# Optimization experiments

Measured on AMD Instinct MI355X. Metric: run time of the kernel, lower is better.

Reference implementation:

```python
import jax, jax.numpy as jnp
import numpy as np

B, T = 8192, 26
V, E, H, L = 23, 100, 128, 64  # vocab, emb dim, GRU hidden, latent; LSTM hidden = E


def setup_inputs() -> dict:
    key = jax.random.key(0)
    ks = jax.random.split(key, 16)
    rn = lambda k, shape, scale=0.1: (jax.random.normal(k, shape, jnp.float32) * scale)
    emb = rn(ks[0], (V, E)).at[0].set(0.0)  # padding_idx=0 row zeroed
    return {
        "z": jax.random.normal(ks[1], (B, L), jnp.float32),
        "x_in": jax.random.randint(ks[2], (B, T), 0, V),
        "emb": emb,
        "fc_z_w": rn(ks[3], (H, L)), "fc_z_b": rn(ks[4], (H,)),
        "gru_wih": rn(ks[5], (3 * H, E)), "gru_whh": rn(ks[6], (3 * H, H)),
        "gru_bih": rn(ks[7], (3 * H,)), "gru_bhh": rn(ks[8], (3 * H,)),
        "lstm_wih": rn(ks[9], (4 * E, H)), "lstm_whh": rn(ks[10], (4 * E, E)),
        "lstm_bih": rn(ks[11], (4 * E,)), "lstm_bhh": rn(ks[12], (4 * E,)),
        "out_w": rn(ks[13], (V, E)), "out_b": rn(ks[14], (V,)),
    }


def _gru(e, h0, Wih, Whh, bih, bhh):
    # e: (B,T,E); precompute input projections for all steps, scan over T.
    xg = jnp.einsum('bti,gi->btg', e, Wih) + bih  # (B,T,3H)

    def step(h, x):
        hg = h @ Whh.T + bhh
        xr, xz, xn = jnp.split(x, 3, axis=-1)
        hr, hz, hn = jnp.split(hg, 3, axis=-1)
        r = jax.nn.sigmoid(xr + hr)
        zg = jax.nn.sigmoid(xz + hz)
        n = jnp.tanh(xn + r * hn)
        h_new = (1.0 - zg) * n + zg * h
        return h_new, h_new

    _, ys = jax.lax.scan(step, h0, jnp.swapaxes(xg, 0, 1))  # (T,B,H)
    return jnp.swapaxes(ys, 0, 1)


def _lstm(x, h0, c0, Wih, Whh, bih, bhh):
    xg = jnp.einsum('bti,gi->btg', x, Wih) + bih  # (B,T,4E)

    def step(hc, xt):
        h, c = hc
        g = xt + h @ Whh.T + bhh
        i, f, gg, o = jnp.split(g, 4, axis=-1)
        c_new = jax.nn.sigmoid(f) * c + jax.nn.sigmoid(i) * jnp.tanh(gg)
        h_new = jax.nn.sigmoid(o) * jnp.tanh(c_new)
        return (h_new, c_new), h_new

    _, ys = jax.lax.scan(step, (h0, c0), jnp.swapaxes(xg, 0, 1))
    return jnp.swapaxes(ys, 0, 1)


def reference(z, x_in, emb, fc_z_w, fc_z_b, gru_wih, gru_whh, gru_bih, gru_bhh,
              lstm_wih, lstm_whh, lstm_bih, lstm_bhh, out_w, out_b):
    h0 = jnp.tanh(z @ fc_z_w.T + fc_z_b)            # (B,H)
    e = emb[x_in]                                    # (B,T,E)
    y = _gru(e, h0, gru_wih, gru_whh, gru_bih, gru_bhh)           # (B,T,H)
    zeros = jnp.zeros((z.shape[0], E), dtype=z.dtype)
    y = _lstm(y, zeros, zeros, lstm_wih, lstm_whh, lstm_bih, lstm_bhh)  # (B,T,E)
    logits = jnp.einsum('bte,ve->btv', y, out_w) + out_b          # (B,T,V)
    return logits
```

## Files before the change

kernel.cpp:

```cpp
#include <hip/hip_runtime.h>
#include <stdint.h>
#include <stddef.h>

#define BB 8192
#define TT 26
#define VV 23
#define EE 100
#define HH 128
#define LL 64

typedef __attribute__((ext_vector_type(8))) short bf16x8;
typedef __attribute__((ext_vector_type(4))) float f32x4;

#define MFMA(a, b, c) __builtin_amdgcn_mfma_f32_16x16x32_bf16((a), (b), (c), 0, 0, 0)

#define OFF_GRUW   0ull
#define OFF_TBL    98304ull
#define OFF_LSTMW  122880ull
#define OFF_OUTW   352256ull
#define OFF_FCZW   360448ull
#define OFF_LBIAS  376832ull

#define L_LW    0
#define L_HF    114688
#define L_LH    131072
#define L_IDX   147456
#define L_TOTAL 148480

__device__ __forceinline__ void force_frag(bf16x8& v) { asm volatile("" : "+v"(v)); }

__device__ __forceinline__ unsigned short f2bf(float f) {
  union { float f; unsigned u; } v; v.f = f;
  unsigned u = v.u;
  return (unsigned short)((u + 0x7FFFu + ((u >> 16) & 1u)) >> 16);
}
__device__ __forceinline__ unsigned short f2bf_fast(float f) {
  union { float f; unsigned u; } v; v.f = f;
  return (unsigned short)((v.u + 0x8000u) >> 16);
}
#define LOG2E 1.4426950408889634f
__device__ __forceinline__ float sigm(float x) {
  return __builtin_amdgcn_rcpf(1.0f + __builtin_amdgcn_exp2f(-x * LOG2E));
}
__device__ __forceinline__ float tanh_(float x) {
  return __builtin_fmaf(-2.0f,
      __builtin_amdgcn_rcpf(1.0f + __builtin_amdgcn_exp2f(x * (2.0f * LOG2E))), 1.0f);
}

__global__ __launch_bounds__(256) void prep_kernel(
    const float* __restrict__ fc_z_w, const float* __restrict__ gru_whh,
    const float* __restrict__ lstm_wih, const float* __restrict__ lstm_whh,
    const float* __restrict__ lstm_bih, const float* __restrict__ lstm_bhh,
    const float* __restrict__ out_w,
    const float* __restrict__ emb, const float* __restrict__ gru_wih,
    const float* __restrict__ gru_bih, const float* __restrict__ gru_bhh,
    char* __restrict__ ws)
{
  __shared__ float emb_s[VV * EE];
  __shared__ float wih_s[16 * EE];
  __shared__ float bih_s[16];
  const int blk = blockIdx.x;
  const int tid = threadIdx.x;

  if (blk >= 690) {
    const int blk2 = blk - 690;
    const int ct   = blk2 >> 1;
    const int half = blk2 & 1;
    const int n0   = ct * 16;

    for (int i = tid; i < VV * EE; i += 256) emb_s[i] = emb[i];
    for (int i = tid; i < 16 * EE; i += 256) wih_s[i] = gru_wih[n0 * EE + i];
    if (tid < 16) bih_s[tid] = gru_bih[n0 + tid];
    __syncthreads();

    const int t512 = half * 256 + tid;
    const int j    = t512 & 7;
    const int lane = (t512 >> 3) & 63;
    const int n16  = lane & 15;
    const int k    = ((lane >> 4) & 3) * 8 + j;
    const int g    = ct >> 3;
    float v = 0.0f;
    if (k < VV) {
      const float* ep = emb_s + k * EE;
      const float* wp = wih_s + n16 * EE;
      float s0 = 0.f, s1 = 0.f, s2 = 0.f, s3 = 0.f;
#pragma unroll 5
      for (int m = 0; m < EE; m += 4) {
        s0 += ep[m] * wp[m];         s1 += ep[m + 1] * wp[m + 1];
        s2 += ep[m + 2] * wp[m + 2]; s3 += ep[m + 3] * wp[m + 3];
      }
      v = bih_s[n16] + ((s0 + s1) + (s2 + s3));
      if (g < 2) v += gru_bhh[g * HH + (ct & 7) * 16 + n16];
    }
    *(unsigned short*)(ws + OFF_TBL + (size_t)(ct * 512 + t512) * 2) = f2bf(v);
    return;
  }

  int e = blk * 256 + tid;

  if (e < 49152) {
    int j = e & 7, lane = (e >> 3) & 63, kc = (e >> 9) & 3, ct = e >> 11;
    int n = ct * 16 + (lane & 15);
    int k = kc * 32 + ((lane >> 4) & 3) * 8 + j;
    *(unsigned short*)(ws + OFF_GRUW + (size_t)e * 2) = f2bf(gru_whh[n * HH + k]);
    return;
  }
  e -= 49152;
  if (e < 114688) {
    int j = e & 7, lane = (e >> 3) & 63, kc = (e >> 9) & 7, ct = e >> 12;
    int row = ct * 16 + (lane & 15);
    int g = row / 112, c = row % 112;
    int q = (lane >> 4) & 3;
    float v = 0.0f;
    if (c < EE) {
      if (kc < 4) {
        int k = kc * 32 + q * 8 + j;
        v = lstm_wih[(g * EE + c) * HH + k];
      } else {
        int k = (kc - 4) * 32 + q * 8 + j;
        if (k < EE) v = lstm_whh[(g * EE + c) * EE + k];
      }
    }
    *(unsigned short*)(ws + OFF_LSTMW + (size_t)e * 2) = f2bf(v);
    return;
  }
  e -= 114688;
  if (e < 4096) {
    int j = e & 7, lane = (e >> 3) & 63, kc = (e >> 9) & 3, ct = e >> 11;
    int n = ct * 16 + (lane & 15);
    int k = kc * 32 + ((lane >> 4) & 3) * 8 + j;
    float v = (n < VV && k < EE) ? out_w[n * EE + k] : 0.0f;
    *(unsigned short*)(ws + OFF_OUTW + (size_t)e * 2) = f2bf(v);
    return;
  }
  e -= 4096;
  if (e < 8192) {
    int j = e & 7, lane = (e >> 3) & 63, kc = (e >> 9) & 1, ct = e >> 10;
    int n = ct * 16 + (lane & 15);
    int k = kc * 32 + ((lane >> 4) & 3) * 8 + j;
    *(unsigned short*)(ws + OFF_FCZW + (size_t)e * 2) = f2bf(fc_z_w[n * LL + k]);
    return;
  }
  e -= 8192;
  if (e < 448) {
    int g = e / 112, c = e % 112;
    float v = (c < EE) ? (lstm_bih[g * EE + c] + lstm_bhh[g * EE + c]) : 0.0f;
    *(float*)(ws + OFF_LBIAS + (size_t)e * 4) = v;
  }
}

__global__ __launch_bounds__(1024, 4) void fused_kernel(
    const float* __restrict__ z, const int* __restrict__ x_in,
    const float* __restrict__ fc_z_b, const float* __restrict__ gru_bhh,
    const unsigned short* __restrict__ gruw, const unsigned short* __restrict__ tbl,
    const unsigned short* __restrict__ fczw,
    const unsigned short* __restrict__ lstmw, const float* __restrict__ lbias,
    const float* __restrict__ out_b, const unsigned short* __restrict__ outw,
    float* __restrict__ out)
{
  extern __shared__ char smem[];
  unsigned short* lwlds = (unsigned short*)(smem + L_LW);
  char*           hfrag = smem + L_HF;
  char*           lhbuf = smem + L_LH;
  unsigned char*  idx_lds = (unsigned char*)(smem + L_IDX);

  const int tid  = threadIdx.x;
  const int wv   = tid >> 6;
  const int lane = tid & 63;
  const int l15  = lane & 15;
  const int q    = (lane >> 4) & 3;
  const int blk  = blockIdx.x;

  for (int i = tid; i < 8192; i += 1024)
    ((unsigned short*)lhbuf)[i] = 0;
  for (int f = tid; f < 7168; f += 1024) {
    int frag_i = f >> 6, within = f & 63;
    int ct = frag_i >> 2, kcl = frag_i & 3;
    *(bf16x8*)((char*)lwlds + (size_t)frag_i * 1024 + within * 16) =
        *(const bf16x8*)(lstmw + ((size_t)(ct * 8 + 4 + kcl)) * 512 + within * 8);
  }

  if (wv < 8) {
    {
      int rid = wv * 64 + lane;
      for (int i = rid; i < TT * 32; i += 512) {
        int t = i >> 5, r = i & 31;
        idx_lds[i] = (unsigned char)x_in[(blk * 32 + r) * TT + t];
      }
    }
    bf16x8 gw[3][4], tw[3];
#pragma unroll
    for (int g = 0; g < 3; g++) {
      int ct = g * 8 + wv;
#pragma unroll
      for (int kc = 0; kc < 4; kc++) {
        gw[g][kc] = *(const bf16x8*)(gruw + (size_t)(ct * 4 + kc) * 512 + lane * 8);
        force_frag(gw[g][kc]);
      }
      tw[g] = *(const bf16x8*)(tbl + (size_t)ct * 512 + lane * 8);
      force_frag(tw[g]);
    }
    const int col = wv * 16 + l15;
    const float b_n = gru_bhh[2 * HH + col];
    const int wbase = (col >> 5) * 512 + ((col >> 3) & 3) * 128 + (col & 7);

    float h[2][4];
    {
      bf16x8 fw0 = *(const bf16x8*)(fczw + (size_t)(wv * 2 + 0) * 512 + lane * 8);
      bf16x8 fw1 = *(const bf16x8*)(fczw + (size_t)(wv * 2 + 1) * 512 + lane * 8);
      float fzb = fc_z_b[col];
#pragma unroll
      for (int mt = 0; mt < 2; mt++) {
        const float* zp = z + (size_t)(blk * 32 + mt * 16 + l15) * LL + q * 8;
        f32x4 z0 = *(const f32x4*)(zp);
        f32x4 z1 = *(const f32x4*)(zp + 4);
        f32x4 z2 = *(const f32x4*)(zp + 32);
        f32x4 z3 = *(const f32x4*)(zp + 36);
        bf16x8 za0, za1;
#pragma unroll
        for (int j = 0; j < 4; j++) {
          za0[j]     = (short)f2bf(z0[j]);
          za0[4 + j] = (short)f2bf(z1[j]);
          za1[j]     = (short)f2bf(z2[j]);
          za1[4 + j] = (short)f2bf(z3[j]);
        }
        f32x4 acc = {fzb, fzb, fzb, fzb};
        acc = MFMA(za0, fw0, acc);
        acc = MFMA(za1, fw1, acc);
#pragma unroll
        for (int i = 0; i < 4; i++) {
          h[mt][i] = tanh_(acc[i]);
          ((unsigned short*)(hfrag + mt * 4096))[wbase + (q * 4 + i) * 8]
              = f2bf_fast(h[mt][i]);
        }
      }
    }
    __syncthreads();

    for (int p = 0; p < TT + 2; p++) {
      if (p < TT) {
#pragma unroll
        for (int mt = 0; mt < 2; mt++) {
          int iv = idx_lds[p * 32 + mt * 16 + l15];
          bf16x8 oh;
#pragma unroll
          for (int j = 0; j < 8; j++)
            oh[j] = (short)((iv == q * 8 + j) ? 0x3F80 : 0);

          f32x4 ar  = {0.0f, 0.0f, 0.0f, 0.0f};
          f32x4 az  = {0.0f, 0.0f, 0.0f, 0.0f};
          f32x4 ahn = {b_n, b_n, b_n, b_n};
          f32x4 axn = {0.0f, 0.0f, 0.0f, 0.0f};
          ar  = MFMA(oh, tw[0], ar);
          az  = MFMA(oh, tw[1], az);
          axn = MFMA(oh, tw[2], axn);

          bf16x8 a[4];
#pragma unroll
          for (int kc = 0; kc < 4; kc++)
            a[kc] = *(const bf16x8*)(hfrag + (p & 1) * 8192 + mt * 4096
                                     + kc * 1024 + lane * 16);
#pragma unroll
          for (int kc = 0; kc < 4; kc++) {
            ar  = MFMA(a[kc], gw[0][kc], ar);
            az  = MFMA(a[kc], gw[1][kc], az);
            ahn = MFMA(a[kc], gw[2][kc], ahn);
          }
#pragma unroll
          for (int i = 0; i < 4; i++) {
            float r  = sigm(ar[i]);
            float zg = sigm(az[i]);
            float n  = tanh_(__builtin_fmaf(r, ahn[i], axn[i]));
            h[mt][i] = __builtin_fmaf(zg, h[mt][i] - n, n);
            ((unsigned short*)(hfrag + ((p + 1) & 1) * 8192 + mt * 4096))
                [wbase + (q * 4 + i) * 8] = f2bf_fast(h[mt][i]);
          }
        }
      }
      __syncthreads();
    }
  } else if (wv < 15) {
    const int tile = wv - 8;
    bf16x8 lwy[4][3];
#pragma unroll
    for (int g = 0; g < 4; g++)
#pragma unroll
      for (int kc = 0; kc < 3; kc++) {
        lwy[g][kc] = *(const bf16x8*)(lstmw + (size_t)((g * 7 + tile) * 8 + kc) * 512 + lane * 8);
        force_frag(lwy[g][kc]);
      }
    const int col = tile * 16 + l15;
    float b[4];
#pragma unroll
    for (int g = 0; g < 4; g++) b[g] = lbias[g * 112 + col];
    const int wbase = (col >> 5) * 512 + ((col >> 3) & 3) * 128 + (col & 7);
    float c[2][4] = {{0, 0, 0, 0}, {0, 0, 0, 0}};
    __syncthreads();

    for (int p = 0; p < TT + 2; p++) {
      if (p >= 1 && p <= TT) {
        bf16x8 yw3[4];
#pragma unroll
        for (int g = 0; g < 4; g++)
          yw3[g] = *(const bf16x8*)(lstmw + (size_t)((g * 7 + tile) * 8 + 3) * 512 + lane * 8);

        f32x4 acc[2][4];
#pragma unroll
        for (int mt = 0; mt < 2; mt++)
#pragma unroll
          for (int g = 0; g < 4; g++) {
            f32x4 ini = {b[g], b[g], b[g], b[g]};
            acc[mt][g] = ini;
          }

#pragma unroll
        for (int kc = 0; kc < 3; kc++) {
          bf16x8 ya0 = *(const bf16x8*)(hfrag + (p & 1) * 8192 + 0 * 4096
                                        + kc * 1024 + lane * 16);
          bf16x8 ya1 = *(const bf16x8*)(hfrag + (p & 1) * 8192 + 1 * 4096
                                        + kc * 1024 + lane * 16);
#pragma unroll
          for (int g = 0; g < 4; g++) {
            acc[0][g] = MFMA(ya0, lwy[g][kc], acc[0][g]);
            acc[1][g] = MFMA(ya1, lwy[g][kc], acc[1][g]);
          }
        }
        {
          bf16x8 ya0 = *(const bf16x8*)(hfrag + (p & 1) * 8192 + 0 * 4096
                                        + 3 * 1024 + lane * 16);
          bf16x8 ya1 = *(const bf16x8*)(hfrag + (p & 1) * 8192 + 1 * 4096
                                        + 3 * 1024 + lane * 16);
#pragma unroll
          for (int g = 0; g < 4; g++) {
            acc[0][g] = MFMA(ya0, yw3[g], acc[0][g]);
            acc[1][g] = MFMA(ya1, yw3[g], acc[1][g]);
          }
        }
#pragma unroll
        for (int kc = 0; kc < 4; kc++) {
          const char* wb = (const char*)lwlds + (size_t)(tile * 4 + kc) * 1024 + lane * 16;
          bf16x8 w0 = *(const bf16x8*)(wb);
          bf16x8 w1 = *(const bf16x8*)(wb + 28672);
          bf16x8 w2 = *(const bf16x8*)(wb + 2 * 28672);
          bf16x8 w3 = *(const bf16x8*)(wb + 3 * 28672);
          bf16x8 ha0 = *(const bf16x8*)(lhbuf + ((p - 1) & 1) * 8192 + 0 * 4096
                                        + kc * 1024 + lane * 16);
          bf16x8 ha1 = *(const bf16x8*)(lhbuf + ((p - 1) & 1) * 8192 + 1 * 4096
                                        + kc * 1024 + lane * 16);
          acc[0][0] = MFMA(ha0, w0, acc[0][0]);
          acc[0][1] = MFMA(ha0, w1, acc[0][1]);
          acc[0][2] = MFMA(ha0, w2, acc[0][2]);
          acc[0][3] = MFMA(ha0, w3, acc[0][3]);
          acc[1][0] = MFMA(ha1, w0, acc[1][0]);
          acc[1][1] = MFMA(ha1, w1, acc[1][1]);
          acc[1][2] = MFMA(ha1, w2, acc[1][2]);
          acc[1][3] = MFMA(ha1, w3, acc[1][3]);
        }
#pragma unroll
        for (int mt = 0; mt < 2; mt++) {
#pragma unroll
          for (int i = 0; i < 4; i++) {
            float ii = sigm(acc[mt][0][i]), ff = sigm(acc[mt][1][i]);
            float gg = tanh_(acc[mt][2][i]), oo = sigm(acc[mt][3][i]);
            float cn = __builtin_fmaf(ff, c[mt][i], ii * gg);
            c[mt][i] = cn;
            ((unsigned short*)(lhbuf + (p & 1) * 8192 + mt * 4096))
                [wbase + (q * 4 + i) * 8] = f2bf_fast(oo * tanh_(cn));
          }
        }
      }
      __syncthreads();
    }
  } else {
    bf16x8 ow[2][4];
#pragma unroll
    for (int ct = 0; ct < 2; ct++)
#pragma unroll
      for (int kc = 0; kc < 4; kc++) {
        ow[ct][kc] = *(const bf16x8*)(outw + (size_t)(ct * 4 + kc) * 512 + lane * 8);
        force_frag(ow[ct][kc]);
      }
    float ob[2];
#pragma unroll
    for (int ct = 0; ct < 2; ct++) {
      int cv = ct * 16 + l15;
      ob[ct] = (cv < VV) ? out_b[cv] : 0.0f;
    }
    __syncthreads();

    for (int p = 0; p < TT + 2; p++) {
      if (p >= 2) {
        const int t = p - 2;
#pragma unroll
        for (int mt = 0; mt < 2; mt++) {
          bf16x8 ha[4];
#pragma unroll
          for (int kc = 0; kc < 4; kc++)
            ha[kc] = *(const bf16x8*)(lhbuf + ((p - 1) & 1) * 8192 + mt * 4096
                                      + kc * 1024 + lane * 16);
#pragma unroll
          for (int ct = 0; ct < 2; ct++) {
            f32x4 acc = {ob[ct], ob[ct], ob[ct], ob[ct]};
#pragma unroll
            for (int kc = 0; kc < 4; kc++)
              acc = MFMA(ha[kc], ow[ct][kc], acc);
            int cv = ct * 16 + l15;
            if (cv < VV) {
#pragma unroll
              for (int i = 0; i < 4; i++) {
                int rowg = blk * 32 + mt * 16 + q * 4 + i;
                out[((size_t)rowg * TT + t) * VV + cv] = acc[i];
              }
            }
          }
        }
      }
      __syncthreads();
    }
  }
}

extern "C" void kernel_launch(void* const* d_in, const int* in_sizes, int n_in,
                              void* d_out, int out_size, void* d_ws, size_t ws_size,
                              hipStream_t stream) {
  (void)in_sizes; (void)n_in; (void)out_size; (void)ws_size;
  const float* z        = (const float*)d_in[0];
  const int*   x_in     = (const int*)  d_in[1];
  const float* emb      = (const float*)d_in[2];
  const float* fc_z_w   = (const float*)d_in[3];
  const float* fc_z_b   = (const float*)d_in[4];
  const float* gru_wih  = (const float*)d_in[5];
  const float* gru_whh  = (const float*)d_in[6];
  const float* gru_bih  = (const float*)d_in[7];
  const float* gru_bhh  = (const float*)d_in[8];
  const float* lstm_wih = (const float*)d_in[9];
  const float* lstm_whh = (const float*)d_in[10];
  const float* lstm_bih = (const float*)d_in[11];
  const float* lstm_bhh = (const float*)d_in[12];
  const float* out_w    = (const float*)d_in[13];
  const float* out_b    = (const float*)d_in[14];
  char*  ws  = (char*)d_ws;
  float* out = (float*)d_out;

  const unsigned short* gruw  = (const unsigned short*)(ws + OFF_GRUW);
  const unsigned short* tblp  = (const unsigned short*)(ws + OFF_TBL);
  const unsigned short* lstmw = (const unsigned short*)(ws + OFF_LSTMW);
  const unsigned short* outw  = (const unsigned short*)(ws + OFF_OUTW);
  const unsigned short* fczw  = (const unsigned short*)(ws + OFF_FCZW);
  const float*          lbias = (const float*)(ws + OFF_LBIAS);

  hipFuncSetAttribute((const void*)fused_kernel,
                      hipFuncAttributeMaxDynamicSharedMemorySize, L_TOTAL);

  prep_kernel<<<738, 256, 0, stream>>>(fc_z_w, gru_whh, lstm_wih, lstm_whh,
                                       lstm_bih, lstm_bhh, out_w,
                                       emb, gru_wih, gru_bih, gru_bhh, ws);
  fused_kernel<<<256, 1024, L_TOTAL, stream>>>(z, x_in, fc_z_b, gru_bhh,
                                               gruw, tblp, fczw, lstmw, lbias,
                                               out_b, outw, out);
}
```

Baseline: 185.9 us.

## Replace per-step block barriers with LDS counters and triple-buffered states

Replaces the per-timestep __syncthreads between the GRU, LSTM and output warp groups with LDS atomic counters (wait/post) and moves the GRU and LSTM hidden-state buffers from double to triple buffering. The aim is to let the pipeline stages drift relative to each other instead of running in lockstep, so one slow stage does not stall every warp. The LSTM y-weights are now held fully in registers, and fewer recurrent-weight fragments are staged in LDS, with the last K chunk read from global memory each step. This adds spin-wait overhead, the risk of a subtle ordering bug, and extra register pressure.

```diff
diff --git a/kernel.cpp b/kernel.cpp
--- a/kernel.cpp
+++ b/kernel.cpp
@@ -22,10 +22,11 @@
 #define OFF_LBIAS  376832ull
 
 #define L_LW    0
-#define L_HF    114688
-#define L_LH    131072
-#define L_IDX   147456
-#define L_TOTAL 148480
+#define L_HF    86016
+#define L_LH    110592
+#define L_IDX   135168
+#define L_CNT   136192
+#define L_TOTAL 136448
 
 __device__ __forceinline__ void force_frag(bf16x8& v) { asm volatile("" : "+v"(v)); }
 
@@ -45,6 +46,17 @@
 __device__ __forceinline__ float tanh_(float x) {
   return __builtin_fmaf(-2.0f,
       __builtin_amdgcn_rcpf(1.0f + __builtin_amdgcn_exp2f(x * (2.0f * LOG2E))), 1.0f);
+}
+
+__device__ __forceinline__ void wait_ge(int* cnt, int tgt) {
+  while (__hip_atomic_load(cnt, __ATOMIC_ACQUIRE, __HIP_MEMORY_SCOPE_WORKGROUP) < tgt)
+    __builtin_amdgcn_s_sleep(2);
+  __builtin_amdgcn_sched_barrier(0);
+}
+__device__ __forceinline__ void post_cnt(int* cnt, int lane) {
+  __threadfence_block();
+  if (lane == 0)
+    __hip_atomic_fetch_add(cnt, 1, __ATOMIC_RELEASE, __HIP_MEMORY_SCOPE_WORKGROUP);
 }
 
 __global__ __launch_bounds__(256) void prep_kernel(
@@ -163,6 +175,10 @@
   char*           hfrag = smem + L_HF;
   char*           lhbuf = smem + L_LH;
   unsigned char*  idx_lds = (unsigned char*)(smem + L_IDX);
+  int*            cnts  = (int*)(smem + L_CNT);
+  int* cg = cnts + 0;
+  int* cl = cnts + 16;
+  int* co = cnts + 32;
 
   const int tid  = threadIdx.x;
   const int wv   = tid >> 6;
@@ -171,11 +187,12 @@
   const int q    = (lane >> 4) & 3;
   const int blk  = blockIdx.x;
 
-  for (int i = tid; i < 8192; i += 1024)
+  if (tid < 48) cnts[tid] = 0;
+  for (int i = tid; i < 12288; i += 1024)
     ((unsigned short*)lhbuf)[i] = 0;
-  for (int f = tid; f < 7168; f += 1024) {
+  for (int f = tid; f < 5376; f += 1024) {
     int frag_i = f >> 6, within = f & 63;
-    int ct = frag_i >> 2, kcl = frag_i & 3;
+    int ct = frag_i / 3, kcl = frag_i % 3;
     *(bf16x8*)((char*)lwlds + (size_t)frag_i * 1024 + within * 16) =
         *(const bf16x8*)(lstmw + ((size_t)(ct * 8 + 4 + kcl)) * 512 + within * 8);
   }
@@ -230,15 +247,20 @@
 #pragma unroll
         for (int i = 0; i < 4; i++) {
           h[mt][i] = tanh_(acc[i]);
-          ((unsigned short*)(hfrag + mt * 4096))[wbase + (q * 4 + i) * 8]
+          ((unsigned short*)(hfrag + 2 * 8192 + mt * 4096))[wbase + (q * 4 + i) * 8]
               = f2bf_fast(h[mt][i]);
         }
       }
     }
     __syncthreads();
 
+#pragma unroll 1
     for (int p = 0; p < TT + 2; p++) {
+      wait_ge(cg, 8 * p);
+      if (p >= 3 && p < TT) wait_ge(cl, 7 * (p - 1));
       if (p < TT) {
+        const int br = (p + 2) % 3;
+        const int bw = (p + 3) % 3;
 #pragma unroll
         for (int mt = 0; mt < 2; mt++) {
           int iv = idx_lds[p * 32 + mt * 16 + l15];
@@ -258,7 +280,7 @@
           bf16x8 a[4];
 #pragma unroll
           for (int kc = 0; kc < 4; kc++)
-            a[kc] = *(const bf16x8*)(hfrag + (p & 1) * 8192 + mt * 4096
+            a[kc] = *(const bf16x8*)(hfrag + br * 8192 + mt * 4096
                                      + kc * 1024 + lane * 16);
 #pragma unroll
           for (int kc = 0; kc < 4; kc++) {
@@ -272,20 +294,20 @@
             float zg = sigm(az[i]);
             float n  = tanh_(__builtin_fmaf(r, ahn[i], axn[i]));
             h[mt][i] = __builtin_fmaf(zg, h[mt][i] - n, n);
-            ((unsigned short*)(hfrag + ((p + 1) & 1) * 8192 + mt * 4096))
+            ((unsigned short*)(hfrag + bw * 8192 + mt * 4096))
                 [wbase + (q * 4 + i) * 8] = f2bf_fast(h[mt][i]);
           }
         }
       }
-      __syncthreads();
+      post_cnt(cg, lane);
     }
   } else if (wv < 15) {
     const int tile = wv - 8;
-    bf16x8 lwy[4][3];
+    bf16x8 lwy[4][4];
 #pragma unroll
     for (int g = 0; g < 4; g++)
 #pragma unroll
-      for (int kc = 0; kc < 3; kc++) {
+      for (int kc = 0; kc < 4; kc++) {
         lwy[g][kc] = *(const bf16x8*)(lstmw + (size_t)((g * 7 + tile) * 8 + kc) * 512 + lane * 8);
         force_frag(lwy[g][kc]);
       }
@@ -297,79 +319,66 @@
     float c[2][4] = {{0, 0, 0, 0}, {0, 0, 0, 0}};
     __syncthreads();
 
+#pragma unroll 1
     for (int p = 0; p < TT + 2; p++) {
+      wait_ge(cl, 7 * p);
       if (p >= 1 && p <= TT) {
-        bf16x8 yw3[4];
-#pragma unroll
-        for (int g = 0; g < 4; g++)
-          yw3[g] = *(const bf16x8*)(lstmw + (size_t)((g * 7 + tile) * 8 + 3) * 512 + lane * 8);
-
-        f32x4 acc[2][4];
-#pragma unroll
-        for (int mt = 0; mt < 2; mt++)
+        wait_ge(cg, 8 * p);
+        if (p >= 4) wait_ge(co, p - 1);
+        const int by = (p + 2) % 3;
+        const int bh = (p + 1) % 3;
+        const int bw2 = (p + 2) % 3;
+#pragma unroll
+        for (int mt = 0; mt < 2; mt++) {
+          f32x4 acc[4];
 #pragma unroll
           for (int g = 0; g < 4; g++) {
             f32x4 ini = {b[g], b[g], b[g], b[g]};
-            acc[mt][g] = ini;
-          }
-
-#pragma unroll
-        for (int kc = 0; kc < 3; kc++) {
-          bf16x8 ya0 = *(const bf16x8*)(hfrag + (p & 1) * 8192 + 0 * 4096
-                                        + kc * 1024 + lane * 16);
-          bf16x8 ya1 = *(const bf16x8*)(hfrag + (p & 1) * 8192 + 1 * 4096
-                                        + kc * 1024 + lane * 16);
-#pragma unroll
-          for (int g = 0; g < 4; g++) {
-            acc[0][g] = MFMA(ya0, lwy[g][kc], acc[0][g]);
-            acc[1][g] = MFMA(ya1, lwy[g][kc], acc[1][g]);
-          }
-        }
-        {
-          bf16x8 ya0 = *(const bf16x8*)(hfrag + (p & 1) * 8192 + 0 * 4096
-                                        + 3 * 1024 + lane * 16);
-          bf16x8 ya1 = *(const bf16x8*)(hfrag + (p & 1) * 8192 + 1 * 4096
-                                        + 3 * 1024 + lane * 16);
-#pragma unroll
-          for (int g = 0; g < 4; g++) {
-            acc[0][g] = MFMA(ya0, yw3[g], acc[0][g]);
-            acc[1][g] = MFMA(ya1, yw3[g], acc[1][g]);
-          }
-        }
-#pragma unroll
-        for (int kc = 0; kc < 4; kc++) {
-          const char* wb = (const char*)lwlds + (size_t)(tile * 4 + kc) * 1024 + lane * 16;
-          bf16x8 w0 = *(const bf16x8*)(wb);
-          bf16x8 w1 = *(const bf16x8*)(wb + 28672);
-          bf16x8 w2 = *(const bf16x8*)(wb + 2 * 28672);
-          bf16x8 w3 = *(const bf16x8*)(wb + 3 * 28672);
-          bf16x8 ha0 = *(const bf16x8*)(lhbuf + ((p - 1) & 1) * 8192 + 0 * 4096
-                                        + kc * 1024 + lane * 16);
-          bf16x8 ha1 = *(const bf16x8*)(lhbuf + ((p - 1) & 1) * 8192 + 1 * 4096
-                                        + kc * 1024 + lane * 16);
-          acc[0][0] = MFMA(ha0, w0, acc[0][0]);
-          acc[0][1] = MFMA(ha0, w1, acc[0][1]);
-          acc[0][2] = MFMA(ha0, w2, acc[0][2]);
-          acc[0][3] = MFMA(ha0, w3, acc[0][3]);
-          acc[1][0] = MFMA(ha1, w0, acc[1][0]);
-          acc[1][1] = MFMA(ha1, w1, acc[1][1]);
-          acc[1][2] = MFMA(ha1, w2, acc[1][2]);
-          acc[1][3] = MFMA(ha1, w3, acc[1][3]);
-        }
-#pragma unroll
-        for (int mt = 0; mt < 2; mt++) {
+            acc[g] = ini;
+          }
+#pragma unroll
+          for (int kc = 0; kc < 4; kc++) {
+            bf16x8 ya = *(const bf16x8*)(hfrag + by * 8192 + mt * 4096
+                                         + kc * 1024 + lane * 16);
+            acc[0] = MFMA(ya, lwy[0][kc], acc[0]);
+            acc[1] = MFMA(ya, lwy[1][kc], acc[1]);
+            acc[2] = MFMA(ya, lwy[2][kc], acc[2]);
+            acc[3] = MFMA(ya, lwy[3][kc], acc[3]);
+          }
+#pragma unroll
+          for (int kc = 0; kc < 4; kc++) {
+            bf16x8 ha = *(const bf16x8*)(lhbuf + bh * 8192 + mt * 4096
+                                         + kc * 1024 + lane * 16);
+            bf16x8 w0, w1, w2, w3;
+            if (kc < 3) {
+              const char* wb = (const char*)lwlds + (size_t)(tile * 3 + kc) * 1024 + lane * 16;
+              w0 = *(const bf16x8*)(wb);
+              w1 = *(const bf16x8*)(wb + 21504);
+              w2 = *(const bf16x8*)(wb + 2 * 21504);
+              w3 = *(const bf16x8*)(wb + 3 * 21504);
+            } else {
+              w0 = *(const bf16x8*)(lstmw + (size_t)((0 * 7 + tile) * 8 + 7) * 512 + lane * 8);
+              w1 = *(const bf16x8*)(lstmw + (size_t)((1 * 7 + tile) * 8 + 7) * 512 + lane * 8);
+              w2 = *(const bf16x8*)(lstmw + (size_t)((2 * 7 + tile) * 8 + 7) * 512 + lane * 8);
+              w3 = *(const bf16x8*)(lstmw + (size_t)((3 * 7 + tile) * 8 + 7) * 512 + lane * 8);
+            }
+            acc[0] = MFMA(ha, w0, acc[0]);
+            acc[1] = MFMA(ha, w1, acc[1]);
+            acc[2] = MFMA(ha, w2, acc[2]);
+            acc[3] = MFMA(ha, w3, acc[3]);
+          }
 #pragma unroll
           for (int i = 0; i < 4; i++) {
-            float ii = sigm(acc[mt][0][i]), ff = sigm(acc[mt][1][i]);
-            float gg = tanh_(acc[mt][2][i]), oo = sigm(acc[mt][3][i]);
+            float ii = sigm(acc[0][i]), ff = sigm(acc[1][i]);
+            float gg = tanh_(acc[2][i]), oo = sigm(acc[3][i]);
             float cn = __builtin_fmaf(ff, c[mt][i], ii * gg);
             c[mt][i] = cn;
-            ((unsigned short*)(lhbuf + (p & 1) * 8192 + mt * 4096))
+            ((unsigned short*)(lhbuf + bw2 * 8192 + mt * 4096))
                 [wbase + (q * 4 + i) * 8] = f2bf_fast(oo * tanh_(cn));
           }
         }
       }
-      __syncthreads();
+      post_cnt(cl, lane);
     }
   } else {
     bf16x8 ow[2][4];
@@ -388,15 +397,18 @@
     }
     __syncthreads();
 
+#pragma unroll 1
     for (int p = 0; p < TT + 2; p++) {
       if (p >= 2) {
+        wait_ge(cl, 7 * p);
+        const int bh = (p + 1) % 3;
         const int t = p - 2;
 #pragma unroll
         for (int mt = 0; mt < 2; mt++) {
           bf16x8 ha[4];
 #pragma unroll
           for (int kc = 0; kc < 4; kc++)
-            ha[kc] = *(const bf16x8*)(lhbuf + ((p - 1) & 1) * 8192 + mt * 4096
+            ha[kc] = *(const bf16x8*)(lhbuf + bh * 8192 + mt * 4096
                                       + kc * 1024 + lane * 16);
 #pragma unroll
           for (int ct = 0; ct < 2; ct++) {
@@ -415,7 +427,7 @@
           }
         }
       }
-      __syncthreads();
+      post_cnt(co, lane);
     }
   }
 }
```

Result: slower. 319.3 us (+71.7%).
